# Kernel tuning notes

Hardware: AMD Instinct MI355X
Metric: run time of the kernel (lower is better)

The kernel has to match this reference:

```python
import math
import jax, jax.numpy as jnp
import numpy as np
from jax.scipy.special import gammaln

BLOCK = 96
GAM = jnp.arange(9801, dtype=jnp.float32) * 0.001 + 0.2  # 0.2 .. 10.0, matches torch.arange(0.2, 10.001, 0.001)
R_GAM = jnp.exp(2.0 * gammaln(2.0 / GAM) - gammaln(1.0 / GAM) - gammaln(3.0 / GAM))

def fspecial_gauss(size, sigma):
    ax = np.arange(size, dtype=np.float64) - (size - 1) / 2.0
    xx, yy = np.meshgrid(ax, ax)
    g = np.exp(-(xx ** 2 + yy ** 2) / (2.0 * sigma ** 2))
    return jnp.asarray(g / g.sum(), dtype=jnp.float32)

GAUSS7 = fspecial_gauss(7, 7.0 / 6.0)

def filter_replicate(img, kernel):
    p = kernel.shape[0] // 2
    x = jnp.pad(img, ((0, 0), (0, 0), (p, p), (p, p)), mode='edge')
    return jax.lax.conv_general_dilated(x, kernel[None, None], (1, 1), 'VALID',
                                        dimension_numbers=('NCHW', 'OIHW', 'NCHW'))

def mscn(img):
    # normalize_img_with_guass, kernel_size=7, sigma=7/6, replicate padding
    mu = filter_replicate(img, GAUSS7)
    sigma = jnp.sqrt(jnp.abs(filter_replicate(img * img, GAUSS7) - mu * mu))
    return (img - mu) / (sigma + 1.0)

def estimate_aggd(x):  # x: [N, npix] -> (alpha, beta_l, beta_r) each [N]
    neg = x < 0
    pos = x > 0
    x2 = x * x
    left_std = jnp.sqrt((x2 * neg).sum(-1) / neg.sum(-1))
    right_std = jnp.sqrt((x2 * pos).sum(-1) / pos.sum(-1))
    gammahat = left_std / right_std
    rhat = jnp.abs(x).mean(-1) ** 2 / x2.mean(-1)
    rhatnorm = rhat * (gammahat ** 3 + 1) * (gammahat + 1) / (gammahat ** 2 + 1) ** 2
    pos_idx = jnp.argmin((R_GAM[None, :] - rhatnorm[:, None]) ** 2, axis=-1)
    alpha = GAM[pos_idx]
    ratio = jnp.exp(0.5 * (gammaln(1.0 / alpha) - gammaln(3.0 / alpha)))
    return alpha, left_std * ratio, right_std * ratio

def compute_feats(blocks):  # [N, bh, bw] -> [N, 18]
    N = blocks.shape[0]
    a0, bl0, br0 = estimate_aggd(blocks.reshape(N, -1))
    feats = [a0, (bl0 + br0) / 2.0]
    for sh in ((0, 1), (1, 0), (1, 1), (1, -1)):
        prod = blocks * jnp.roll(blocks, sh, axis=(1, 2))
        a, bl, br = estimate_aggd(prod.reshape(N, -1))
        mean = (br - bl) * jnp.exp(gammaln(2.0 / a) - gammaln(1.0 / a))
        feats += [a, mean, bl, br]
    return jnp.stack(feats, axis=-1)

def _cubic_np(x):
    ax = np.abs(x); ax2 = ax * ax; ax3 = ax2 * ax
    return ((1.5 * ax3 - 2.5 * ax2 + 1) * (ax <= 1)
            + (-0.5 * ax3 + 2.5 * ax2 - 4 * ax + 2) * ((ax > 1) & (ax <= 2)))

def _resize_params(in_len, scale):  # MATLAB imresize weights/indices (antialiased cubic)
    out_len = int(in_len * scale)
    kw = 4.0 / scale
    u = np.arange(1, out_len + 1) / scale + 0.5 * (1 - 1 / scale)
    left = np.floor(u - kw / 2)
    P = int(math.ceil(kw)) + 2
    idx = left[:, None] + np.arange(P)[None, :]
    w = scale * _cubic_np(scale * (u[:, None] - idx))
    w = w / w.sum(1, keepdims=True)
    i0 = idx - 1  # 0-based; symmetric reflection at borders
    i0 = np.where(i0 < 0, -i0 - 1, i0)
    i0 = np.where(i0 >= in_len, 2 * in_len - i0 - 1, i0)
    return jnp.asarray(w, jnp.float32), jnp.asarray(i0.astype(np.int32))

def imresize_half(img):  # MATLAB-style bicubic, antialiasing=True, scale=0.5; h first then w
    h, w = img.shape[2], img.shape[3]
    wh, ih = _resize_params(h, 0.5)
    img = jnp.einsum('bchpw,hp->bchw', jnp.take(img, ih, axis=2), wh)
    ww, iw = _resize_params(w, 0.5)
    img = jnp.einsum('bchwp,wp->bchw', jnp.take(img, iw, axis=3), ww)
    return img

def _to_blocks(x, bs):  # [b,1,H,W] -> [b*nh*nw, bs, bs] (consistent ordering across scales)
    b, _, H, W = x.shape
    nh, nw = H // bs, W // bs
    x = x.reshape(b, nh, bs, nw, bs).transpose(0, 1, 3, 2, 4)
    return x.reshape(b * nh * nw, bs, bs)

def niqe_metric(img, mu_pris, cov_pris):
    b, _, h, w = img.shape
    nbh, nbw = h // BLOCK, w // BLOCK
    img = img[..., : nbh * BLOCK, : nbw * BLOCK]
    dist = []
    for scale in (1, 2):
        norm = mscn(img)
        feats = compute_feats(_to_blocks(norm, BLOCK // scale))
        dist.append(feats.reshape(b, nbh * nbw, 18))
        if scale == 1:
            img = imresize_half(img / 255.0) * 255.0
    dist = jnp.concatenate(dist, axis=-1)  # [b, nblocks, 36]
    mu_dist = dist.mean(axis=1)
    xc = dist - mu_dist[:, None, :]
    cov_dist = jnp.einsum('bnf,bng->bfg', xc, xc) / (dist.shape[1] - 1)
    invcov = jnp.linalg.pinv((cov_pris + cov_dist) / 2.0)
    diff = mu_pris - mu_dist
    q = jnp.einsum('bf,bfg,bg->b', diff, invcov, diff)
    return jnp.sqrt(q)

def setup_inputs():
    key = jax.random.key(0)
    k1, k2, k3 = jax.random.split(key, 3)
    b = 4
    x = jax.random.uniform(k1, (b, 3, 1080, 1920), dtype=jnp.float32)
    mu_pris_param = jax.random.normal(k2, (b, 36), dtype=jnp.float32) * 0.5
    A = jax.random.normal(k3, (b, 36, 36), dtype=jnp.float32) * 0.1
    cov_pris_param = jnp.einsum('bij,bkj->bik', A, A) + 1e-3 * jnp.eye(36, dtype=jnp.float32)
    return {"x": x, "mu_pris_param": mu_pris_param, "cov_pris_param": cov_pris_param}

def reference(x, mu_pris_param, cov_pris_param):
    # NIQE.forward: RGB [0,1] -> Y channel (YIQ luma) scaled to [0,255], rounded
    y = (0.299 * x[:, 0] + 0.587 * x[:, 1] + 0.114 * x[:, 2]) * 255.0
    y = jnp.round(y)
    return niqe_metric(y[:, None], mu_pris_param, cov_pris_param)
```

## Files before the change

kernel.cpp:

```cpp
#include <hip/hip_runtime.h>
#include <math.h>

#define NB   4
#define H1   1056
#define W1   1920
#define H2   528
#define W2   960
#define NBLK 220
#define NBW  20
#define NF   36
#define NGAM 9801
#define NSL1 4
#define NPART (NB * NBLK * NSL1 + NB * NBLK)

__device__ __forceinline__ int reflect_idx(int i, int n) {
    if (i < 0) return -i - 1;
    if (i >= n) return 2 * n - i - 1;
    return i;
}

__global__ void k_gray_rgam(const float4* __restrict__ x, float4* __restrict__ y,
                            float* __restrict__ rg, float* __restrict__ rt,
                            float* __restrict__ mf) {
    const int W4 = W1 / 4;
    const int gtotal = NB * H1 * W4;
    int idx = blockIdx.x * 256 + threadIdx.x;
    if (idx < gtotal) {
        int w4 = idx % W4;
        int t  = idx / W4;
        int h  = t % H1;
        int b  = t / H1;
        size_t base = ((size_t)(b * 3) * 1080 + h) * W4 + w4;
        float4 r  = x[base];
        float4 g  = x[base + (size_t)1080 * W4];
        float4 bb = x[base + (size_t)2 * 1080 * W4];
        float4 o;
        o.x = rintf((0.299f * r.x + 0.587f * g.x + 0.114f * bb.x) * 255.0f);
        o.y = rintf((0.299f * r.y + 0.587f * g.y + 0.114f * bb.y) * 255.0f);
        o.z = rintf((0.299f * r.z + 0.587f * g.z + 0.114f * bb.z) * 255.0f);
        o.w = rintf((0.299f * r.w + 0.587f * g.w + 0.114f * bb.w) * 255.0f);
        y[idx] = o;
    } else {
        int i = idx - gtotal;
        if (i < NGAM) {
            float g = (float)i * 0.001f + 0.2f;
            float l1 = lgammaf(1.0f / g);
            float l2 = lgammaf(2.0f / g);
            float l3 = lgammaf(3.0f / g);
            rg[i] = expf(2.0f * l2 - l1 - l3);
            rt[i] = expf(0.5f * (l1 - l3));
            mf[i] = expf(l2 - l1);
        }
    }
}

__global__ __launch_bounds__(256) void k_mscn(const float* __restrict__ src,
                                              float* __restrict__ out, int H, int W) {
    __shared__ float tile[38][40];
    __shared__ float h1s[38][36];
    __shared__ float h2s[38][36];
    __shared__ float gw1[8];

    int tx = threadIdx.x;
    int ty = threadIdx.y;
    int tid = ty * 32 + tx;

    if (tid < 7) {
        double s = 7.0 / 6.0;
        double sum = 0.0;
        #pragma unroll
        for (int k = 0; k < 7; k++) sum += exp(-(double)((k - 3) * (k - 3)) / (2.0 * s * s));
        double e = exp(-(double)((tid - 3) * (tid - 3)) / (2.0 * s * s));
        gw1[tid] = (float)(e / sum);
    }

    int b = blockIdx.z;
    const float* p = src + (size_t)b * H * W;
    int ox0 = blockIdx.x * 32, oy0 = blockIdx.y * 32;

    for (int t = tid; t < 38 * 38; t += 256) {
        int r = t / 38, c = t % 38;
        int gr = oy0 - 3 + r; gr = gr < 0 ? 0 : (gr >= H ? H - 1 : gr);
        int gc = ox0 - 3 + c; gc = gc < 0 ? 0 : (gc >= W ? W - 1 : gc);
        tile[r][c] = p[(size_t)gr * W + gc];
    }
    __syncthreads();

    for (int t = tid; t < 38 * 8; t += 256) {
        int r = t / 8, c0 = (t % 8) * 4;
        float4 f0 = *(const float4*)&tile[r][c0];
        float4 f1 = *(const float4*)&tile[r][c0 + 4];
        float2 f2 = *(const float2*)&tile[r][c0 + 8];
        float v[10] = {f0.x, f0.y, f0.z, f0.w, f1.x, f1.y, f1.z, f1.w, f2.x, f2.y};
        float s1[4] = {0, 0, 0, 0}, s2[4] = {0, 0, 0, 0};
        #pragma unroll
        for (int k = 0; k < 7; k++) {
            float w = gw1[k];
            #pragma unroll
            for (int s = 0; s < 4; s++) {
                float vv = v[s + k];
                s1[s] += w * vv;
                s2[s] += w * vv * vv;
            }
        }
        *(float4*)&h1s[r][c0] = make_float4(s1[0], s1[1], s1[2], s1[3]);
        *(float4*)&h2s[r][c0] = make_float4(s2[0], s2[1], s2[2], s2[3]);
    }
    __syncthreads();

    int ly0 = ty * 4;
    float a1[10], a2[10];
    #pragma unroll
    for (int k = 0; k < 10; k++) { a1[k] = h1s[ly0 + k][tx]; a2[k] = h2s[ly0 + k][tx]; }
    float* q = out + (size_t)b * H * W;
    #pragma unroll
    for (int s = 0; s < 4; s++) {
        int oy = oy0 + ly0 + s, ox = ox0 + tx;
        if (oy < H) {
            float m1 = 0.0f, m2 = 0.0f;
            #pragma unroll
            for (int k = 0; k < 7; k++) {
                float w = gw1[k];
                m1 += w * a1[s + k];
                m2 += w * a2[s + k];
            }
            float sig = sqrtf(fabsf(m2 - m1 * m1));
            q[(size_t)oy * W + ox] = (tile[ly0 + s + 3][tx + 3] - m1) / (sig + 1.0f);
        }
    }
}

__device__ const float RW8[8] = {-0.01171875f, -0.03515625f, 0.11328125f, 0.43359375f,
                                  0.43359375f,  0.11328125f, -0.03515625f, -0.01171875f};

__global__ __launch_bounds__(256) void k_resize(const float* __restrict__ y,
                                                float* __restrict__ half) {
    __shared__ float yt[70][72];
    __shared__ float vv[32][72];
    int tid = threadIdx.y * 32 + threadIdx.x;
    int b = blockIdx.z;
    int j0 = blockIdx.x * 32, i0 = blockIdx.y * 32;
    const float* py = y + (size_t)b * H1 * W1;
    int rbase = 2 * i0 - 3, cbase = 2 * j0 - 3;

    for (int t = tid; t < 70 * 70; t += 256) {
        int r = t / 70, c = t % 70;
        int gr = reflect_idx(rbase + r, H1);
        int gc = reflect_idx(cbase + c, W1);
        yt[r][c] = py[(size_t)gr * W1 + gc] / 255.0f;
    }
    __syncthreads();

    for (int t = tid; t < 32 * 70; t += 256) {
        int i = t / 70, c = t % 70;
        float acc = 0.0f;
        #pragma unroll
        for (int p = 0; p < 8; p++) acc += RW8[p] * yt[2 * i + p][c];
        vv[i][c] = acc;
    }
    __syncthreads();

    float* ph = half + (size_t)b * H2 * W2;
    for (int t = tid; t < 1024; t += 256) {
        int i = t >> 5, j = t & 31;
        int oy = i0 + i, ox = j0 + j;
        if (oy < H2 && ox < W2) {
            float acc = 0.0f;
            #pragma unroll
            for (int p = 0; p < 8; p++) acc += RW8[p] * vv[i][2 * j + p];
            ph[(size_t)oy * W2 + ox] = acc * 255.0f;
        }
    }
}

template <int CW>
__device__ __forceinline__ void loadv(float* d, const float* s) {
    float4 v = *(const float4*)s;
    d[0] = v.x; d[1] = v.y; d[2] = v.z; d[3] = v.w;
}

template <int COLS, int TPR>
__device__ __forceinline__ void fpart_body(const float* __restrict__ p, int W,
                                           int row0, int BSfull,
                                           float* __restrict__ outp) {
    constexpr int SPAN = 12, CW = 4, NCH = 3;
    __shared__ float wls[3][25];
    int tid = threadIdx.x, lane = tid & 63, wv = tid >> 6;

    int li = tid / TPR;
    int c0 = (tid % TPR) * SPAN;
    int gi = row0 + li;
    int gim = (gi == 0) ? BSfull - 1 : gi - 1;
    const float* rowcp = p + (size_t)gi * W;
    const float* rowmp = p + (size_t)gim * W;

    float c2 = rowcp[c0 == 0 ? COLS - 1 : c0 - 1];
    float m2 = rowmp[c0 == 0 ? COLS - 1 : c0 - 1];
    float mrightE = rowmp[c0 + SPAN == COLS ? 0 : c0 + SPAN];

    float sn[5] = {0, 0, 0, 0, 0}, s2[5] = {0, 0, 0, 0, 0}, sa[5] = {0, 0, 0, 0, 0};
    int cneg[5] = {0, 0, 0, 0, 0}, cnz[5] = {0, 0, 0, 0, 0};

    auto PROC = [&](float v0, float cl, float up, float ul, float ur) {
        float v[5] = {v0, v0 * cl, v0 * up, v0 * ul, v0 * ur};
        #pragma unroll
        for (int s = 0; s < 5; s++) {
            float vv = v[s];
            float t = fminf(vv, 0.0f);
            sn[s] += t * t;
            s2[s] += vv * vv;
            sa[s] += fabsf(vv);
            cneg[s] += (int)__popcll(__ballot(vv < 0.0f));
            cnz[s]  += (int)__popcll(__ballot(vv != 0.0f));
        }
    };

    float c1 = 0.0f, m1 = 0.0f;
    #pragma unroll
    for (int j = 0; j < NCH; j++) {
        float cc[CW], mm[CW];
        loadv<CW>(cc, rowcp + c0 + j * CW);
        #pragma unroll
        for (int k = 0; k < CW; k++) mm[k] = __shfl_up(cc[k], TPR, 64);
        if (lane < TPR) loadv<CW>(mm, rowmp + c0 + j * CW);
        #pragma unroll
        for (int k = 0; k < CW; k++) {
            if (j == 0 && k == 0) { c1 = cc[0]; m1 = mm[0]; }
            else {
                PROC(c1, c2, m1, m2, mm[k]);
                c2 = c1; m2 = m1; c1 = cc[k]; m1 = mm[k];
            }
        }
    }
    PROC(c1, c2, m1, m2, mrightE);

    #pragma unroll
    for (int s = 0; s < 5; s++) {
        float vals[3] = {sn[s], s2[s], sa[s]};
        const int rows3[3] = {0, 1, 4};
        #pragma unroll
        for (int m = 0; m < 3; m++) {
            float v = vals[m];
            #pragma unroll
            for (int off = 32; off > 0; off >>= 1) v += __shfl_down(v, off, 64);
            if (lane == 0) wls[wv][s * 5 + rows3[m]] = v;
        }
        if (lane == 0) {
            wls[wv][s * 5 + 2] = (float)cneg[s];
            wls[wv][s * 5 + 3] = (float)cnz[s];
        }
    }
    __syncthreads();
    if (tid < 25) outp[tid] = wls[0][tid] + wls[1][tid] + wls[2][tid];
}

__global__ __launch_bounds__(192) void k_fpart(const float* __restrict__ nrm1,
                                               const float* __restrict__ nrm2,
                                               float* __restrict__ part) {
    int sg = blockIdx.x;
    if (sg < NB * NBLK * NSL1) {
        int g = sg >> 2, sl = sg & 3;
        int b = g / NBLK, r = g % NBLK;
        const float* p = nrm1 + (size_t)b * H1 * W1 + (size_t)(r / NBW * 96) * W1
                       + (size_t)(r % NBW) * 96;
        fpart_body<96, 8>(p, W1, sl * 24, 96, part + (size_t)sg * 25);
    } else {
        int g = sg - NB * NBLK * NSL1;
        int b = g / NBLK, r = g % NBLK;
        const float* p = nrm2 + (size_t)b * H2 * W2 + (size_t)(r / NBW * 48) * W2
                       + (size_t)(r % NBW) * 48;
        fpart_body<48, 4>(p, W2, 0, 48, part + (size_t)sg * 25);
    }
}

__global__ __launch_bounds__(64) void k_ffinal(const float* __restrict__ part,
                                               const float* __restrict__ rgam,
                                               const float* __restrict__ ratio_t,
                                               const float* __restrict__ meanfac_t,
                                               float* __restrict__ feats) {
    __shared__ float ss[25];
    __shared__ float srn[5], sls[5], srs[5];
    int g = blockIdx.x, lane = threadIdx.x;
    int FOFF, BS;
    if (g < NB * NBLK) {
        if (lane < 25) {
            float s = 0.0f;
            #pragma unroll
            for (int sl = 0; sl < NSL1; sl++)
                s += part[(size_t)(g * NSL1 + sl) * 25 + lane];
            ss[lane] = s;
        }
        FOFF = 0; BS = 96;
    } else {
        if (lane < 25) ss[lane] = part[(size_t)(NB * NBLK * NSL1 + (g - NB * NBLK)) * 25 + lane];
        FOFF = 18; BS = 48;
    }
    __syncthreads();

    if (lane < 5) {
        int s = lane;
        float SN  = ss[s * 5 + 0];
        float S2  = ss[s * 5 + 1];
        float CN  = ss[s * 5 + 2];
        float CNZ = ss[s * 5 + 3];
        float SA  = ss[s * 5 + 4];
        float SP = S2 - SN;
        float CP = CNZ - CN;
        float ls = sqrtf(SN / CN);
        float rs = sqrtf(SP / CP);
        float gh = ls / rs;
        float Nn = (float)(BS * BS);
        float am = SA / Nn;
        float rhat = (am * am) / (S2 / Nn);
        float g2 = gh * gh;
        float rn = rhat * (g2 * gh + 1.0f) * (gh + 1.0f) / ((g2 + 1.0f) * (g2 + 1.0f));
        srn[s] = rn; sls[s] = ls; srs[s] = rs;
    }
    __syncthreads();

    int gl = (g < NB * NBLK) ? g : g - NB * NBLK;
    float* fp = feats + (size_t)gl * NF + FOFF;
    for (int s = 0; s < 5; s++) {
        float rn = srn[s];
        int lo = -1, hi = NGAM;
        while (hi - lo > 1) {
            int n = hi - lo - 1;
            int stride = n / 65 + 1;
            int pi = lo + (lane + 1) * stride;
            bool valid = pi < hi;
            float v = valid ? rgam[pi] : 0.0f;
            unsigned long long blw = __ballot(valid && (v < rn));
            int k = __popcll(blw);
            int oldlo = lo;
            lo = oldlo + k * stride;
            int cand = oldlo + (k + 1) * stride;
            if (cand < hi) hi = cand;
        }
        int lb = hi;
        int ix;
        if (lb <= 0) ix = 0;
        else if (lb >= NGAM) ix = NGAM - 1;
        else {
            float dl = rgam[lb - 1] - rn, dr = rgam[lb] - rn;
            ix = (dl * dl <= dr * dr) ? lb - 1 : lb;
        }
        if (lane == 0) {
            float a = (float)ix * 0.001f + 0.2f;
            float ratio = ratio_t[ix];
            float bl = sls[s] * ratio;
            float br = srs[s] * ratio;
            if (s == 0) {
                fp[0] = a; fp[1] = 0.5f * (bl + br);
            } else {
                float mn = (br - bl) * meanfac_t[ix];
                int base = 2 + (s - 1) * 4;
                fp[base] = a; fp[base + 1] = mn; fp[base + 2] = bl; fp[base + 3] = br;
            }
        }
    }
}

__global__ __launch_bounds__(256) void k_stats(const float* __restrict__ feats,
                                               const float* __restrict__ mu_pris,
                                               const float* __restrict__ cov_pris,
                                               float* __restrict__ out) {
    __shared__ float dist[NBLK * NF];
    __shared__ __align__(16) float distT[NF][228];
    __shared__ float mu[NF];
    __shared__ float M[NF][NF + 1];
    __shared__ float facs[NF];
    __shared__ float dd[NF];

    int b = blockIdx.x, tid = threadIdx.x;
    for (int t = tid; t < NBLK * NF; t += 256) dist[t] = feats[(size_t)b * NBLK * NF + t];
    __syncthreads();
    if (tid < NF) {
        float s = 0.0f;
        for (int n = 0; n < NBLK; n++) s += dist[n * NF + tid];
        mu[tid] = s / (float)NBLK;
    }
    __syncthreads();
    for (int t = tid; t < NF * NBLK; t += 256) {
        int f = t / NBLK, n = t % NBLK;
        distT[f][n] = dist[n * NF + f] - mu[f];
    }
    __syncthreads();

    if (tid < 144) {
        int f0 = (tid / 12) * 3, g0 = (tid % 12) * 3;
        float acc[3][3] = {{0,0,0},{0,0,0},{0,0,0}};
        for (int n = 0; n < NBLK; n += 4) {
            float4 A[3], B[3];
            #pragma unroll
            for (int i = 0; i < 3; i++) A[i] = *(const float4*)&distT[f0 + i][n];
            #pragma unroll
            for (int j = 0; j < 3; j++) B[j] = *(const float4*)&distT[g0 + j][n];
            #pragma unroll
            for (int i = 0; i < 3; i++)
                #pragma unroll
                for (int j = 0; j < 3; j++)
                    acc[i][j] += A[i].x * B[j].x + A[i].y * B[j].y
                               + A[i].z * B[j].z + A[i].w * B[j].w;
        }
        const float* cp = cov_pris + (size_t)b * NF * NF;
        #pragma unroll
        for (int i = 0; i < 3; i++)
            #pragma unroll
            for (int j = 0; j < 3; j++) {
                int f = f0 + i, gg = g0 + j;
                M[f][gg] = (cp[f * NF + gg] + acc[i][j] / (float)(NBLK - 1)) * 0.5f;
            }
    }
    if (tid < NF) {
        float d = mu_pris[b * NF + tid] - mu[tid];
        dd[tid] = d;
        M[tid][NF] = d;
    }
    __syncthreads();

    for (int k = 0; k < NF; k++) {
        if (tid < NF && tid != k) facs[tid] = M[tid][k] / M[k][k];
        __syncthreads();
        for (int t = tid; t < NF * (NF + 1); t += 256) {
            int i = t / (NF + 1), j = t % (NF + 1);
            if (i != k && j > k) M[i][j] -= facs[i] * M[k][j];
        }
        __syncthreads();
    }

    if (tid < 64) {
        double c = (tid < NF) ? (double)dd[tid] * ((double)M[tid][NF] / (double)M[tid][tid]) : 0.0;
        #pragma unroll
        for (int off = 32; off > 0; off >>= 1) c += __shfl_down(c, off, 64);
        if (tid == 0) out[b] = (float)sqrt(c);
    }
}

extern "C" void kernel_launch(void* const* d_in, const int* in_sizes, int n_in,
                              void* d_out, int out_size, void* d_ws, size_t ws_size,
                              hipStream_t stream) {
    const float* x        = (const float*)d_in[0];
    const float* mu_pris  = (const float*)d_in[1];
    const float* cov_pris = (const float*)d_in[2];
    float* out = (float*)d_out;
    float* ws  = (float*)d_ws;

    float* y     = ws;
    float* nrm   = y + (size_t)NB * H1 * W1;
    float* half  = nrm + (size_t)NB * H1 * W1;
    float* nrm2  = half + (size_t)NB * H2 * W2;
    float* rgam  = nrm2 + (size_t)NB * H2 * W2;
    float* ratio = rgam + NGAM;
    float* mfac  = ratio + NGAM;
    float* feats = mfac + NGAM;
    float* part  = feats + (size_t)NB * NBLK * NF;

    const int NGB = NB * H1 * (W1 / 4);
    k_gray_rgam<<<(NGB + NGAM + 255) / 256, 256, 0, stream>>>(
        (const float4*)x, (float4*)y, rgam, ratio, mfac);

    dim3 thr(32, 8);
    k_mscn<<<dim3(W1 / 32, H1 / 32, NB), thr, 0, stream>>>(y, nrm, H1, W1);
    k_resize<<<dim3(W2 / 32, (H2 + 31) / 32, NB), thr, 0, stream>>>(y, half);
    k_mscn<<<dim3(W2 / 32, (H2 + 31) / 32, NB), thr, 0, stream>>>(half, nrm2, H2, W2);

    k_fpart<<<NPART, 192, 0, stream>>>(nrm, nrm2, part);
    k_ffinal<<<2 * NB * NBLK, 64, 0, stream>>>(part, rgam, ratio, mfac, feats);

    k_stats<<<NB, 256, 0, stream>>>(feats, mu_pris, cov_pris, out);
}
```

Before: 165.1 us.

## Merge mscn and resize launches and fuse feature finalization into fpart

The full-resolution MSCN and the 2x resize now run as one launch whose block index picks the work, with shared memory reused through a union-like buffer. Feature finalization (the AGGD gamma search) moves into k_fpart: each slice writes its partial sums, bumps a per-block atomic counter, and the last slice to finish reduces the partials and computes the features. This removes two kernel launches and the separate k_ffinal pass, in exchange for atomics, fences and counters that must be zeroed each call (done in the gray kernel). The fused resize/mscn launch also forces both paths to share one shared-memory size, which can lower occupancy.

```diff
diff --git a/kernel.cpp b/kernel.cpp
--- a/kernel.cpp
+++ b/kernel.cpp
@@ -11,7 +11,15 @@
 #define NF   36
 #define NGAM 9801
 #define NSL1 4
+#define NCNT (NB * NBLK)
 #define NPART (NB * NBLK * NSL1 + NB * NBLK)
+
+#define MS_BX (W1 / 32)
+#define MS_BY (H1 / 32)
+#define MS_NB (MS_BX * MS_BY * NB)
+#define RS_BX (W2 / 32)
+#define RS_BY ((H2 + 31) / 32)
+#define RS_NB (RS_BX * RS_BY * NB)
 
 __device__ __forceinline__ int reflect_idx(int i, int n) {
     if (i < 0) return -i - 1;
@@ -21,7 +29,7 @@
 
 __global__ void k_gray_rgam(const float4* __restrict__ x, float4* __restrict__ y,
                             float* __restrict__ rg, float* __restrict__ rt,
-                            float* __restrict__ mf) {
+                            float* __restrict__ mf, int* __restrict__ cnt) {
     const int W4 = W1 / 4;
     const int gtotal = NB * H1 * W4;
     int idx = blockIdx.x * 256 + threadIdx.x;
@@ -50,52 +58,55 @@
             rg[i] = expf(2.0f * l2 - l1 - l3);
             rt[i] = expf(0.5f * (l1 - l3));
             mf[i] = expf(l2 - l1);
-        }
-    }
-}
-
-__global__ __launch_bounds__(256) void k_mscn(const float* __restrict__ src,
-                                              float* __restrict__ out, int H, int W) {
-    __shared__ float tile[38][40];
-    __shared__ float h1s[38][36];
-    __shared__ float h2s[38][36];
-    __shared__ float gw1[8];
-
-    int tx = threadIdx.x;
-    int ty = threadIdx.y;
-    int tid = ty * 32 + tx;
-
+        } else if (i < NGAM + NCNT) {
+            cnt[i - NGAM] = 0;
+        }
+    }
+}
+
+struct MscnS {
+    float tile[38][40];
+    float h1s[38][36];
+    float h2s[38][36];
+    float gw1[8];
+};
+struct ResizeS {
+    float yt[70][72];
+    float vv[32][72];
+};
+
+__device__ __forceinline__ void mscn_body(const float* __restrict__ src,
+                                          float* __restrict__ out, int H, int W,
+                                          int ox0, int oy0, int b,
+                                          int tx, int ty, int tid, MscnS& S) {
     if (tid < 7) {
         double s = 7.0 / 6.0;
         double sum = 0.0;
         #pragma unroll
         for (int k = 0; k < 7; k++) sum += exp(-(double)((k - 3) * (k - 3)) / (2.0 * s * s));
         double e = exp(-(double)((tid - 3) * (tid - 3)) / (2.0 * s * s));
-        gw1[tid] = (float)(e / sum);
-    }
-
-    int b = blockIdx.z;
+        S.gw1[tid] = (float)(e / sum);
+    }
+
     const float* p = src + (size_t)b * H * W;
-    int ox0 = blockIdx.x * 32, oy0 = blockIdx.y * 32;
-
     for (int t = tid; t < 38 * 38; t += 256) {
         int r = t / 38, c = t % 38;
         int gr = oy0 - 3 + r; gr = gr < 0 ? 0 : (gr >= H ? H - 1 : gr);
         int gc = ox0 - 3 + c; gc = gc < 0 ? 0 : (gc >= W ? W - 1 : gc);
-        tile[r][c] = p[(size_t)gr * W + gc];
+        S.tile[r][c] = p[(size_t)gr * W + gc];
     }
     __syncthreads();
 
     for (int t = tid; t < 38 * 8; t += 256) {
         int r = t / 8, c0 = (t % 8) * 4;
-        float4 f0 = *(const float4*)&tile[r][c0];
-        float4 f1 = *(const float4*)&tile[r][c0 + 4];
-        float2 f2 = *(const float2*)&tile[r][c0 + 8];
+        float4 f0 = *(const float4*)&S.tile[r][c0];
+        float4 f1 = *(const float4*)&S.tile[r][c0 + 4];
+        float2 f2 = *(const float2*)&S.tile[r][c0 + 8];
         float v[10] = {f0.x, f0.y, f0.z, f0.w, f1.x, f1.y, f1.z, f1.w, f2.x, f2.y};
         float s1[4] = {0, 0, 0, 0}, s2[4] = {0, 0, 0, 0};
         #pragma unroll
         for (int k = 0; k < 7; k++) {
-            float w = gw1[k];
+            float w = S.gw1[k];
             #pragma unroll
             for (int s = 0; s < 4; s++) {
                 float vv = v[s + k];
@@ -103,15 +114,15 @@
                 s2[s] += w * vv * vv;
             }
         }
-        *(float4*)&h1s[r][c0] = make_float4(s1[0], s1[1], s1[2], s1[3]);
-        *(float4*)&h2s[r][c0] = make_float4(s2[0], s2[1], s2[2], s2[3]);
+        *(float4*)&S.h1s[r][c0] = make_float4(s1[0], s1[1], s1[2], s1[3]);
+        *(float4*)&S.h2s[r][c0] = make_float4(s2[0], s2[1], s2[2], s2[3]);
     }
     __syncthreads();
 
     int ly0 = ty * 4;
     float a1[10], a2[10];
     #pragma unroll
-    for (int k = 0; k < 10; k++) { a1[k] = h1s[ly0 + k][tx]; a2[k] = h2s[ly0 + k][tx]; }
+    for (int k = 0; k < 10; k++) { a1[k] = S.h1s[ly0 + k][tx]; a2[k] = S.h2s[ly0 + k][tx]; }
     float* q = out + (size_t)b * H * W;
     #pragma unroll
     for (int s = 0; s < 4; s++) {
@@ -120,12 +131,12 @@
             float m1 = 0.0f, m2 = 0.0f;
             #pragma unroll
             for (int k = 0; k < 7; k++) {
-                float w = gw1[k];
+                float w = S.gw1[k];
                 m1 += w * a1[s + k];
                 m2 += w * a2[s + k];
             }
             float sig = sqrtf(fabsf(m2 - m1 * m1));
-            q[(size_t)oy * W + ox] = (tile[ly0 + s + 3][tx + 3] - m1) / (sig + 1.0f);
+            q[(size_t)oy * W + ox] = (S.tile[ly0 + s + 3][tx + 3] - m1) / (sig + 1.0f);
         }
     }
 }
@@ -133,13 +144,9 @@
 __device__ const float RW8[8] = {-0.01171875f, -0.03515625f, 0.11328125f, 0.43359375f,
                                   0.43359375f,  0.11328125f, -0.03515625f, -0.01171875f};
 
-__global__ __launch_bounds__(256) void k_resize(const float* __restrict__ y,
-                                                float* __restrict__ half) {
-    __shared__ float yt[70][72];
-    __shared__ float vv[32][72];
-    int tid = threadIdx.y * 32 + threadIdx.x;
-    int b = blockIdx.z;
-    int j0 = blockIdx.x * 32, i0 = blockIdx.y * 32;
+__device__ __forceinline__ void resize_body(const float* __restrict__ y,
+                                            float* __restrict__ half,
+                                            int j0, int i0, int b, int tid, ResizeS& S) {
     const float* py = y + (size_t)b * H1 * W1;
     int rbase = 2 * i0 - 3, cbase = 2 * j0 - 3;
 
@@ -147,7 +154,7 @@
         int r = t / 70, c = t % 70;
         int gr = reflect_idx(rbase + r, H1);
         int gc = reflect_idx(cbase + c, W1);
-        yt[r][c] = py[(size_t)gr * W1 + gc] / 255.0f;
+        S.yt[r][c] = py[(size_t)gr * W1 + gc] / 255.0f;
     }
     __syncthreads();
 
@@ -155,8 +162,8 @@
         int i = t / 70, c = t % 70;
         float acc = 0.0f;
         #pragma unroll
-        for (int p = 0; p < 8; p++) acc += RW8[p] * yt[2 * i + p][c];
-        vv[i][c] = acc;
+        for (int p = 0; p < 8; p++) acc += RW8[p] * S.yt[2 * i + p][c];
+        S.vv[i][c] = acc;
     }
     __syncthreads();
 
@@ -167,25 +174,51 @@
         if (oy < H2 && ox < W2) {
             float acc = 0.0f;
             #pragma unroll
-            for (int p = 0; p < 8; p++) acc += RW8[p] * vv[i][2 * j + p];
+            for (int p = 0; p < 8; p++) acc += RW8[p] * S.vv[i][2 * j + p];
             ph[(size_t)oy * W2 + ox] = acc * 255.0f;
         }
     }
 }
 
-template <int CW>
-__device__ __forceinline__ void loadv(float* d, const float* s) {
-    float4 v = *(const float4*)s;
-    d[0] = v.x; d[1] = v.y; d[2] = v.z; d[3] = v.w;
+__global__ __launch_bounds__(256) void k_ms_rs(const float* __restrict__ y,
+                                               float* __restrict__ nrm,
+                                               float* __restrict__ half) {
+    __shared__ __align__(16) char smem[sizeof(ResizeS)];
+    int bid = blockIdx.x;
+    int tid = threadIdx.x;
+    int tx = tid & 31, ty = tid >> 5;
+    if (bid < MS_NB) {
+        int bx = bid % MS_BX;
+        int t  = bid / MS_BX;
+        int by = t % MS_BY;
+        int b  = t / MS_BY;
+        mscn_body(y, nrm, H1, W1, bx * 32, by * 32, b, tx, ty, tid,
+                  *reinterpret_cast<MscnS*>(smem));
+    } else {
+        int rid = bid - MS_NB;
+        int jx = rid % RS_BX;
+        int t  = rid / RS_BX;
+        int iy = t % RS_BY;
+        int b  = t / RS_BY;
+        resize_body(y, half, jx * 32, iy * 32, b, tid,
+                    *reinterpret_cast<ResizeS*>(smem));
+    }
+}
+
+__global__ __launch_bounds__(256) void k_mscn2(const float* __restrict__ src,
+                                               float* __restrict__ out) {
+    __shared__ MscnS S;
+    int tid = threadIdx.x;
+    mscn_body(src, out, H2, W2, blockIdx.x * 32, blockIdx.y * 32, blockIdx.z,
+              tid & 31, tid >> 5, tid, S);
 }
 
 template <int COLS, int TPR>
 __device__ __forceinline__ void fpart_body(const float* __restrict__ p, int W,
                                            int row0, int BSfull,
-                                           float* __restrict__ outp) {
+                                           int tid, float wls[3][25]) {
     constexpr int SPAN = 12, CW = 4, NCH = 3;
-    __shared__ float wls[3][25];
-    int tid = threadIdx.x, lane = tid & 63, wv = tid >> 6;
+    int lane = tid & 63, wv = tid >> 6;
 
     int li = tid / TPR;
     int c0 = (tid % TPR) * SPAN;
@@ -219,10 +252,16 @@
     #pragma unroll
     for (int j = 0; j < NCH; j++) {
         float cc[CW], mm[CW];
-        loadv<CW>(cc, rowcp + c0 + j * CW);
+        {
+            float4 v = *(const float4*)(rowcp + c0 + j * CW);
+            cc[0] = v.x; cc[1] = v.y; cc[2] = v.z; cc[3] = v.w;
+        }
         #pragma unroll
         for (int k = 0; k < CW; k++) mm[k] = __shfl_up(cc[k], TPR, 64);
-        if (lane < TPR) loadv<CW>(mm, rowmp + c0 + j * CW);
+        if (lane < TPR) {
+            float4 v = *(const float4*)(rowmp + c0 + j * CW);
+            mm[0] = v.x; mm[1] = v.y; mm[2] = v.z; mm[3] = v.w;
+        }
         #pragma unroll
         for (int k = 0; k < CW; k++) {
             if (j == 0 && k == 0) { c1 = cc[0]; m1 = mm[0]; }
@@ -250,55 +289,16 @@
             wls[wv][s * 5 + 3] = (float)cnz[s];
         }
     }
-    __syncthreads();
-    if (tid < 25) outp[tid] = wls[0][tid] + wls[1][tid] + wls[2][tid];
-}
-
-__global__ __launch_bounds__(192) void k_fpart(const float* __restrict__ nrm1,
-                                               const float* __restrict__ nrm2,
-                                               float* __restrict__ part) {
-    int sg = blockIdx.x;
-    if (sg < NB * NBLK * NSL1) {
-        int g = sg >> 2, sl = sg & 3;
-        int b = g / NBLK, r = g % NBLK;
-        const float* p = nrm1 + (size_t)b * H1 * W1 + (size_t)(r / NBW * 96) * W1
-                       + (size_t)(r % NBW) * 96;
-        fpart_body<96, 8>(p, W1, sl * 24, 96, part + (size_t)sg * 25);
-    } else {
-        int g = sg - NB * NBLK * NSL1;
-        int b = g / NBLK, r = g % NBLK;
-        const float* p = nrm2 + (size_t)b * H2 * W2 + (size_t)(r / NBW * 48) * W2
-                       + (size_t)(r % NBW) * 48;
-        fpart_body<48, 4>(p, W2, 0, 48, part + (size_t)sg * 25);
-    }
-}
-
-__global__ __launch_bounds__(64) void k_ffinal(const float* __restrict__ part,
+}
+
+__device__ __forceinline__ void finalize_feats(int tid, int BS, const float* ss,
+                                               float* srn, float* sls, float* srs,
                                                const float* __restrict__ rgam,
                                                const float* __restrict__ ratio_t,
                                                const float* __restrict__ meanfac_t,
-                                               float* __restrict__ feats) {
-    __shared__ float ss[25];
-    __shared__ float srn[5], sls[5], srs[5];
-    int g = blockIdx.x, lane = threadIdx.x;
-    int FOFF, BS;
-    if (g < NB * NBLK) {
-        if (lane < 25) {
-            float s = 0.0f;
-            #pragma unroll
-            for (int sl = 0; sl < NSL1; sl++)
-                s += part[(size_t)(g * NSL1 + sl) * 25 + lane];
-            ss[lane] = s;
-        }
-        FOFF = 0; BS = 96;
-    } else {
-        if (lane < 25) ss[lane] = part[(size_t)(NB * NBLK * NSL1 + (g - NB * NBLK)) * 25 + lane];
-        FOFF = 18; BS = 48;
-    }
-    __syncthreads();
-
-    if (lane < 5) {
-        int s = lane;
+                                               float* __restrict__ fp) {
+    if (tid < 5) {
+        int s = tid;
         float SN  = ss[s * 5 + 0];
         float S2  = ss[s * 5 + 1];
         float CN  = ss[s * 5 + 2];
@@ -317,46 +317,100 @@
         srn[s] = rn; sls[s] = ls; srs[s] = rs;
     }
     __syncthreads();
-
-    int gl = (g < NB * NBLK) ? g : g - NB * NBLK;
-    float* fp = feats + (size_t)gl * NF + FOFF;
-    for (int s = 0; s < 5; s++) {
-        float rn = srn[s];
-        int lo = -1, hi = NGAM;
-        while (hi - lo > 1) {
-            int n = hi - lo - 1;
-            int stride = n / 65 + 1;
-            int pi = lo + (lane + 1) * stride;
-            bool valid = pi < hi;
-            float v = valid ? rgam[pi] : 0.0f;
-            unsigned long long blw = __ballot(valid && (v < rn));
-            int k = __popcll(blw);
-            int oldlo = lo;
-            lo = oldlo + k * stride;
-            int cand = oldlo + (k + 1) * stride;
-            if (cand < hi) hi = cand;
-        }
-        int lb = hi;
-        int ix;
-        if (lb <= 0) ix = 0;
-        else if (lb >= NGAM) ix = NGAM - 1;
-        else {
-            float dl = rgam[lb - 1] - rn, dr = rgam[lb] - rn;
-            ix = (dl * dl <= dr * dr) ? lb - 1 : lb;
-        }
-        if (lane == 0) {
-            float a = (float)ix * 0.001f + 0.2f;
-            float ratio = ratio_t[ix];
-            float bl = sls[s] * ratio;
-            float br = srs[s] * ratio;
-            if (s == 0) {
-                fp[0] = a; fp[1] = 0.5f * (bl + br);
-            } else {
-                float mn = (br - bl) * meanfac_t[ix];
-                int base = 2 + (s - 1) * 4;
-                fp[base] = a; fp[base + 1] = mn; fp[base + 2] = bl; fp[base + 3] = br;
-            }
-        }
+    if (tid < 64) {
+        int lane = tid;
+        for (int s = 0; s < 5; s++) {
+            float rn = srn[s];
+            int lo = -1, hi = NGAM;
+            while (hi - lo > 1) {
+                int n = hi - lo - 1;
+                int stride = n / 65 + 1;
+                int pi = lo + (lane + 1) * stride;
+                bool valid = pi < hi;
+                float v = valid ? rgam[pi] : 0.0f;
+                unsigned long long blw = __ballot(valid && (v < rn));
+                int k = __popcll(blw);
+                int oldlo = lo;
+                lo = oldlo + k * stride;
+                int cand = oldlo + (k + 1) * stride;
+                if (cand < hi) hi = cand;
+            }
+            int lb = hi;
+            int ix;
+            if (lb <= 0) ix = 0;
+            else if (lb >= NGAM) ix = NGAM - 1;
+            else {
+                float dl = rgam[lb - 1] - rn, dr = rgam[lb] - rn;
+                ix = (dl * dl <= dr * dr) ? lb - 1 : lb;
+            }
+            if (lane == 0) {
+                float a = (float)ix * 0.001f + 0.2f;
+                float ratio = ratio_t[ix];
+                float bl = sls[s] * ratio;
+                float br = srs[s] * ratio;
+                if (s == 0) {
+                    fp[0] = a; fp[1] = 0.5f * (bl + br);
+                } else {
+                    float mn = (br - bl) * meanfac_t[ix];
+                    int base = 2 + (s - 1) * 4;
+                    fp[base] = a; fp[base + 1] = mn; fp[base + 2] = bl; fp[base + 3] = br;
+                }
+            }
+        }
+    }
+}
+
+__global__ __launch_bounds__(192) void k_fpart(const float* __restrict__ nrm1,
+                                               const float* __restrict__ nrm2,
+                                               float* __restrict__ part,
+                                               int* __restrict__ cnt,
+                                               const float* __restrict__ rgam,
+                                               const float* __restrict__ ratio_t,
+                                               const float* __restrict__ meanfac_t,
+                                               float* __restrict__ feats) {
+    __shared__ float wls[3][25];
+    __shared__ float ss[25];
+    __shared__ float srn[5], sls[5], srs[5];
+    __shared__ int dofin;
+    int sg = blockIdx.x, tid = threadIdx.x;
+
+    if (sg < NB * NBLK * NSL1) {
+        int g = sg >> 2, sl = sg & 3;
+        int b = g / NBLK, r = g % NBLK;
+        const float* p = nrm1 + (size_t)b * H1 * W1 + (size_t)(r / NBW * 96) * W1
+                       + (size_t)(r % NBW) * 96;
+        fpart_body<96, 8>(p, W1, sl * 24, 96, tid, wls);
+        __syncthreads();
+        if (tid < 25) {
+            atomicExch(&part[(size_t)sg * 25 + tid], wls[0][tid] + wls[1][tid] + wls[2][tid]);
+            __threadfence();
+        }
+        __syncthreads();
+        if (tid == 0) dofin = (atomicAdd(&cnt[g], 1) == NSL1 - 1) ? 1 : 0;
+        __syncthreads();
+        if (!dofin) return;
+        __threadfence();
+        if (tid < 25) {
+            float s = 0.0f;
+            #pragma unroll
+            for (int sl2 = 0; sl2 < NSL1; sl2++)
+                s += atomicAdd(&part[(size_t)(g * NSL1 + sl2) * 25 + tid], 0.0f);
+            ss[tid] = s;
+        }
+        __syncthreads();
+        finalize_feats(tid, 96, ss, srn, sls, srs, rgam, ratio_t, meanfac_t,
+                       feats + (size_t)g * NF + 0);
+    } else {
+        int g = sg - NB * NBLK * NSL1;
+        int b = g / NBLK, r = g % NBLK;
+        const float* p = nrm2 + (size_t)b * H2 * W2 + (size_t)(r / NBW * 48) * W2
+                       + (size_t)(r % NBW) * 48;
+        fpart_body<48, 4>(p, W2, 0, 48, tid, wls);
+        __syncthreads();
+        if (tid < 25) ss[tid] = wls[0][tid] + wls[1][tid] + wls[2][tid];
+        __syncthreads();
+        finalize_feats(tid, 48, ss, srn, sls, srs, rgam, ratio_t, meanfac_t,
+                       feats + (size_t)g * NF + 18);
     }
 }
 
@@ -454,18 +508,17 @@
     float* mfac  = ratio + NGAM;
     float* feats = mfac + NGAM;
     float* part  = feats + (size_t)NB * NBLK * NF;
+    int*   cnt   = (int*)(part + (size_t)NPART * 25);
 
     const int NGB = NB * H1 * (W1 / 4);
-    k_gray_rgam<<<(NGB + NGAM + 255) / 256, 256, 0, stream>>>(
-        (const float4*)x, (float4*)y, rgam, ratio, mfac);
-
-    dim3 thr(32, 8);
-    k_mscn<<<dim3(W1 / 32, H1 / 32, NB), thr, 0, stream>>>(y, nrm, H1, W1);
-    k_resize<<<dim3(W2 / 32, (H2 + 31) / 32, NB), thr, 0, stream>>>(y, half);
-    k_mscn<<<dim3(W2 / 32, (H2 + 31) / 32, NB), thr, 0, stream>>>(half, nrm2, H2, W2);
-
-    k_fpart<<<NPART, 192, 0, stream>>>(nrm, nrm2, part);
-    k_ffinal<<<2 * NB * NBLK, 64, 0, stream>>>(part, rgam, ratio, mfac, feats);
+    k_gray_rgam<<<(NGB + NGAM + NCNT + 255) / 256, 256, 0, stream>>>(
+        (const float4*)x, (float4*)y, rgam, ratio, mfac, cnt);
+
+    k_ms_rs<<<MS_NB + RS_NB, 256, 0, stream>>>(y, nrm, half);
+
+    k_mscn2<<<dim3(RS_BX, RS_BY, NB), 256, 0, stream>>>(half, nrm2);
+
+    k_fpart<<<NPART, 192, 0, stream>>>(nrm, nrm2, part, cnt, rgam, ratio, mfac, feats);
 
     k_stats<<<NB, 256, 0, stream>>>(feats, mu_pris, cov_pris, out);
 }
```

Result: slower. 336.3 us (+103.7%).
